# Performance work log

Measured on AMD Instinct MI355X. Metric: run time of the kernel, lower is better.

Reference implementation:

```python
import jax, jax.numpy as jnp
import numpy as np
from jax import lax

IN, H1, H2, OUT = 256, 512, 512, 1
T, B = 2048, 64


def lstm_layer(x, W_ih, W_hh, b_ih, b_hh):
    # x: (T, B, I); W_ih: (4H, I); W_hh: (4H, H); biases: (4H,)
    H = W_hh.shape[1]
    # precompute input contribution for all timesteps (one big GEMM)
    xg = jnp.einsum('tbi,gi->tbg', x, W_ih) + b_ih + b_hh  # (T, B, 4H)

    def step(carry, xg_t):
        h, c = carry
        gates = xg_t + h @ W_hh.T  # (B, 4H), PyTorch gate order i,f,g,o
        i, f, g, o = jnp.split(gates, 4, axis=-1)
        c = jax.nn.sigmoid(f) * c + jax.nn.sigmoid(i) * jnp.tanh(g)
        h = jax.nn.sigmoid(o) * jnp.tanh(c)
        return (h, c), h

    h0 = jnp.zeros((x.shape[1], H), x.dtype)
    _, hs = lax.scan(step, (h0, h0), xg)
    return hs  # (T, B, H)


def setup_inputs() -> dict:
    key = jax.random.key(0)
    ks = jax.random.split(key, 11)
    s1 = 1.0 / np.sqrt(H1)
    s2 = 1.0 / np.sqrt(H2)
    inp = {
        'input': jax.random.normal(ks[0], (T, B, IN), jnp.float32),
        'W_ih1': jax.random.uniform(ks[1], (4 * H1, IN), jnp.float32, -s1, s1),
        'W_hh1': jax.random.uniform(ks[2], (4 * H1, H1), jnp.float32, -s1, s1),
        'b_ih1': jax.random.uniform(ks[3], (4 * H1,), jnp.float32, -s1, s1),
        'b_hh1': jax.random.uniform(ks[4], (4 * H1,), jnp.float32, -s1, s1),
        'W_ih2': jax.random.uniform(ks[5], (4 * H2, H1), jnp.float32, -s2, s2),
        'W_hh2': jax.random.uniform(ks[6], (4 * H2, H2), jnp.float32, -s2, s2),
        'b_ih2': jax.random.uniform(ks[7], (4 * H2,), jnp.float32, -s2, s2),
        'b_hh2': jax.random.uniform(ks[8], (4 * H2,), jnp.float32, -s2, s2),
        'W_out': jax.random.uniform(ks[9], (OUT, H2), jnp.float32, -s2, s2),
        'b_out': jax.random.uniform(ks[10], (OUT,), jnp.float32, -s2, s2),
    }
    return inp


def reference(input, W_ih1, W_hh1, b_ih1, b_hh1, W_ih2, W_hh2, b_ih2, b_hh2, W_out, b_out):
    h1 = lstm_layer(input, W_ih1, W_hh1, b_ih1, b_hh1)   # (T, B, H1)
    h2 = lstm_layer(h1, W_ih2, W_hh2, b_ih2, b_hh2)      # (T, B, H2)
    out = jnp.einsum('tbh,oh->tbo', h2, W_out) + b_out   # (T, B, OUT)
    return jax.nn.sigmoid(out)
```

## Files before the change

kernel.cpp:

```cpp
#include <hip/hip_runtime.h>
#include <math.h>

#define T_STEPS 2048
#define BATCH   64
#define HDIM    512
#define GDIM    2048
#define INDIM   256
#define NBLK_RE 128
#define HB_STEP (HDIM * BATCH)

typedef _Float16 f16x8 __attribute__((ext_vector_type(8)));
typedef _Float16 f16x4 __attribute__((ext_vector_type(4)));
typedef float    f32x4 __attribute__((ext_vector_type(4)));

__device__ __forceinline__ float sigf(float x) { return 1.0f / (1.0f + __expf(-x)); }
__device__ __forceinline__ float tanh_fast(float x) {
    return 1.0f - 2.0f / (__expf(2.0f * x) + 1.0f);
}

__global__ __launch_bounds__(256) void cvt_f16(const float* __restrict__ src,
                                               _Float16* __restrict__ dst, int n4)
{
    int i = blockIdx.x * 256 + threadIdx.x;
    if (i < n4) {
        float4 v = ((const float4*)src)[i];
        f16x4 h;
        h[0] = (_Float16)v.x; h[1] = (_Float16)v.y;
        h[2] = (_Float16)v.z; h[3] = (_Float16)v.w;
        ((f16x4*)dst)[i] = h;
    }
}

__device__ __forceinline__ void wait_flags(const unsigned* __restrict__ flags,
                                           unsigned tgt, int tid)
{
    for (;;) {
        unsigned f = tgt;
        if (tid < NBLK_RE)
            f = __hip_atomic_load(flags + (size_t)tid * 16,
                                  __ATOMIC_RELAXED, __HIP_MEMORY_SCOPE_AGENT);
        if (__syncthreads_and((int)(f >= tgt))) break;
    }
    __atomic_signal_fence(__ATOMIC_ACQUIRE);
}

__global__ __launch_bounds__(256, 1) void lstm_fused(
    const _Float16* __restrict__ xh,
    const _Float16* __restrict__ Wf1h,
    const _Float16* __restrict__ Wf1i,
    const _Float16* __restrict__ Wf2i,
    const _Float16* __restrict__ Wf2h,
    const float* __restrict__ bih1, const float* __restrict__ bhh1,
    const float* __restrict__ bih2, const float* __restrict__ bhh2,
    _Float16* __restrict__ hb1,
    _Float16* __restrict__ hb2,
    float* __restrict__ c1,
    float* __restrict__ c2,
    unsigned* __restrict__ flag1,
    unsigned* __restrict__ flag2,
    int nsteps, unsigned t0a)
{
    __shared__ float    gl[16][68];
    __shared__ _Float16 hsm[64][4];

    const int tid   = threadIdx.x;
    const int layer = blockIdx.x >> 7;
    const int wg    = blockIdx.x & (NBLK_RE - 1);
    const int j0    = wg * 4;
    const int wv    = tid >> 6;
    const int ln    = tid & 63;
    const int l16   = ln & 15;
    const int quad  = ln >> 4;
    const int grow  = (l16 >> 2) * HDIM + j0 + (l16 & 3);
    const int du    = wv;
    const int bu    = tid & 63;
    const int dd    = j0 + du;

    if (layer == 0) {
        f16x8 Bh[16], Bx[8];
#pragma unroll
        for (int j = 0; j < 16; j++) {
            const uint4 u = *(const uint4*)&Wf1h[(size_t)grow * HDIM + j * 32 + quad * 8];
            Bh[j] = __builtin_bit_cast(f16x8, u);
        }
#pragma unroll
        for (int j = 0; j < 8; j++) {
            const uint4 u = *(const uint4*)&Wf1i[(size_t)grow * INDIM + j * 32 + quad * 8];
            Bx[j] = __builtin_bit_cast(f16x8, u);
        }
        float c_reg = c1[(size_t)dd * BATCH + bu];
        const float bi_ = bih1[0 * HDIM + dd] + bhh1[0 * HDIM + dd];
        const float bf_ = bih1[1 * HDIM + dd] + bhh1[1 * HDIM + dd];
        const float bg_ = bih1[2 * HDIM + dd] + bhh1[2 * HDIM + dd];
        const float bo_ = bih1[3 * HDIM + dd] + bhh1[3 * HDIM + dd];

        for (int t = 0; t < nsteps; t++) {
            f32x4 acc0 = {0.f, 0.f, 0.f, 0.f}, acc1 = {0.f, 0.f, 0.f, 0.f};

            {
                const _Float16* xp = xh + ((size_t)t * BATCH + 16 * wv + l16) * INDIM
                                   + quad * 8;
                ulonglong2 ax[8];
#pragma unroll
                for (int j = 0; j < 8; j++)
                    ax[j] = *(const ulonglong2*)(xp + j * 32);
#pragma unroll
                for (int j = 0; j < 8; j += 2) {
                    acc0 = __builtin_amdgcn_mfma_f32_16x16x32_f16(
                        __builtin_bit_cast(f16x8, ax[j]),     Bx[j],     acc0, 0, 0, 0);
                    acc1 = __builtin_amdgcn_mfma_f32_16x16x32_f16(
                        __builtin_bit_cast(f16x8, ax[j + 1]), Bx[j + 1], acc1, 0, 0, 0);
                }
            }

            wait_flags(flag1, t0a + (unsigned)t, tid);
            {
                const _Float16* hp = hb1 + (size_t)t * HB_STEP
                                   + (size_t)(16 * wv + l16) * HDIM + quad * 8;
                ulonglong2 a[16];
#pragma unroll
                for (int j = 0; j < 16; j++)
                    a[j] = *(const ulonglong2*)(hp + j * 32);
#pragma unroll
                for (int j = 0; j < 16; j += 2) {
                    acc0 = __builtin_amdgcn_mfma_f32_16x16x32_f16(
                        __builtin_bit_cast(f16x8, a[j]),     Bh[j],     acc0, 0, 0, 0);
                    acc1 = __builtin_amdgcn_mfma_f32_16x16x32_f16(
                        __builtin_bit_cast(f16x8, a[j + 1]), Bh[j + 1], acc1, 0, 0, 0);
                }
            }
            f32x4 d = acc0 + acc1;
            *(f32x4*)&gl[l16][16 * wv + quad * 4] = d;
            __syncthreads();

            {
                float si = gl[4 * 0 + du][bu] + bi_;
                float sf = gl[4 * 1 + du][bu] + bf_;
                float sg = gl[4 * 2 + du][bu] + bg_;
                float so = gl[4 * 3 + du][bu] + bo_;
                c_reg = sigf(sf) * c_reg + sigf(si) * tanh_fast(sg);
                float h = sigf(so) * tanh_fast(c_reg);
                hsm[bu][du] = (_Float16)h;
            }
            __syncthreads();

            if (tid < 64) {
                unsigned long long pk = *(const unsigned long long*)&hsm[tid][0];
                unsigned long long* dst = (unsigned long long*)
                    (hb1 + (size_t)(t + 1) * HB_STEP + (size_t)tid * HDIM + j0);
                __hip_atomic_store(dst, pk, __ATOMIC_RELAXED, __HIP_MEMORY_SCOPE_AGENT);
                if (t == nsteps - 1) {
                    unsigned long long* dst0 = (unsigned long long*)
                        (hb1 + (size_t)tid * HDIM + j0);
                    __hip_atomic_store(dst0, pk, __ATOMIC_RELAXED, __HIP_MEMORY_SCOPE_AGENT);
                }
                if (tid == 0) {
                    asm volatile("s_waitcnt vmcnt(0)" ::: "memory");
                    __hip_atomic_store(flag1 + (size_t)wg * 16, t0a + (unsigned)t + 1u,
                                       __ATOMIC_RELAXED, __HIP_MEMORY_SCOPE_AGENT);
                }
            }
        }
        c1[(size_t)dd * BATCH + bu] = c_reg;
    } else {
        f16x8 Bh[16], Bi[16];
#pragma unroll
        for (int j = 0; j < 16; j++) {
            const uint4 uh = *(const uint4*)&Wf2h[(size_t)grow * HDIM + j * 32 + quad * 8];
            Bh[j] = __builtin_bit_cast(f16x8, uh);
            const uint4 ui = *(const uint4*)&Wf2i[(size_t)grow * HDIM + j * 32 + quad * 8];
            Bi[j] = __builtin_bit_cast(f16x8, ui);
        }
        float c_reg = c2[(size_t)dd * BATCH + bu];
        const float bi_ = bih2[0 * HDIM + dd] + bhh2[0 * HDIM + dd];
        const float bf_ = bih2[1 * HDIM + dd] + bhh2[1 * HDIM + dd];
        const float bg_ = bih2[2 * HDIM + dd] + bhh2[2 * HDIM + dd];
        const float bo_ = bih2[3 * HDIM + dd] + bhh2[3 * HDIM + dd];

        for (int t = 0; t < nsteps; t++) {
            f32x4 acc0 = {0.f, 0.f, 0.f, 0.f}, acc1 = {0.f, 0.f, 0.f, 0.f};

            wait_flags(flag1, t0a + (unsigned)t + 1u, tid);
            {
                const _Float16* hp = hb1 + (size_t)(t + 1) * HB_STEP
                                   + (size_t)(16 * wv + l16) * HDIM + quad * 8;
                ulonglong2 a[16];
#pragma unroll
                for (int j = 0; j < 16; j++)
                    a[j] = *(const ulonglong2*)(hp + j * 32);
#pragma unroll
                for (int j = 0; j < 16; j += 2) {
                    acc0 = __builtin_amdgcn_mfma_f32_16x16x32_f16(
                        __builtin_bit_cast(f16x8, a[j]),     Bi[j],     acc0, 0, 0, 0);
                    acc1 = __builtin_amdgcn_mfma_f32_16x16x32_f16(
                        __builtin_bit_cast(f16x8, a[j + 1]), Bi[j + 1], acc1, 0, 0, 0);
                }
            }

            wait_flags(flag2, t0a + (unsigned)t, tid);
            {
                const _Float16* hp = hb2 + (size_t)t * HB_STEP
                                   + (size_t)(16 * wv + l16) * HDIM + quad * 8;
                ulonglong2 a[16];
#pragma unroll
                for (int j = 0; j < 16; j++)
                    a[j] = *(const ulonglong2*)(hp + j * 32);
#pragma unroll
                for (int j = 0; j < 16; j += 2) {
                    acc0 = __builtin_amdgcn_mfma_f32_16x16x32_f16(
                        __builtin_bit_cast(f16x8, a[j]),     Bh[j],     acc0, 0, 0, 0);
                    acc1 = __builtin_amdgcn_mfma_f32_16x16x32_f16(
                        __builtin_bit_cast(f16x8, a[j + 1]), Bh[j + 1], acc1, 0, 0, 0);
                }
            }
            f32x4 d = acc0 + acc1;
            *(f32x4*)&gl[l16][16 * wv + quad * 4] = d;
            __syncthreads();

            {
                float si = gl[4 * 0 + du][bu] + bi_;
                float sf = gl[4 * 1 + du][bu] + bf_;
                float sg = gl[4 * 2 + du][bu] + bg_;
                float so = gl[4 * 3 + du][bu] + bo_;
                c_reg = sigf(sf) * c_reg + sigf(si) * tanh_fast(sg);
                float h = sigf(so) * tanh_fast(c_reg);
                hsm[bu][du] = (_Float16)h;
            }
            __syncthreads();

            if (tid < 64) {
                unsigned long long pk = *(const unsigned long long*)&hsm[tid][0];
                unsigned long long* dst = (unsigned long long*)
                    (hb2 + (size_t)(t + 1) * HB_STEP + (size_t)tid * HDIM + j0);
                __hip_atomic_store(dst, pk, __ATOMIC_RELAXED, __HIP_MEMORY_SCOPE_AGENT);
                if (t == nsteps - 1) {
                    unsigned long long* dst0 = (unsigned long long*)
                        (hb2 + (size_t)tid * HDIM + j0);
                    __hip_atomic_store(dst0, pk, __ATOMIC_RELAXED, __HIP_MEMORY_SCOPE_AGENT);
                }
                if (tid == 0) {
                    asm volatile("s_waitcnt vmcnt(0)" ::: "memory");
                    __hip_atomic_store(flag2 + (size_t)wg * 16, t0a + (unsigned)t + 1u,
                                       __ATOMIC_RELAXED, __HIP_MEMORY_SCOPE_AGENT);
                }
            }
        }
        c2[(size_t)dd * BATCH + bu] = c_reg;
    }
}

__global__ __launch_bounds__(256) void out_kernel(
    const _Float16* __restrict__ h2, const float* __restrict__ Wout,
    const float* __restrict__ bout, float* __restrict__ out)
{
    const int t = blockIdx.x;
    const int q = threadIdx.x >> 6, b = threadIdx.x & 63;
    const _Float16* base = &h2[(size_t)t * HB_STEP + (size_t)b * HDIM];
    float s = 0.0f;
#pragma unroll 8
    for (int k = q * 128; k < q * 128 + 128; k += 4) {
        const uint2 u = *(const uint2*)&base[k];
        f16x4 h = __builtin_bit_cast(f16x4, u);
        s += Wout[k] * (float)h[0] + Wout[k + 1] * (float)h[1]
           + Wout[k + 2] * (float)h[2] + Wout[k + 3] * (float)h[3];
    }
    __shared__ float red[4][64];
    red[q][b] = s;
    __syncthreads();
    if (q == 0) {
        float v = red[0][b] + red[1][b] + red[2][b] + red[3][b] + bout[0];
        out[t * BATCH + b] = sigf(v);
    }
}

static size_t req_bytes(int C) {
    return 65536
         + 2ull * HDIM * BATCH * 4
         + 3ull * GDIM * HDIM * 2
         + (size_t)GDIM * INDIM * 2
         + (size_t)T_STEPS * BATCH * INDIM * 2
         + 2ull * (size_t)(C + 1) * BATCH * HDIM * 2;
}

extern "C" void kernel_launch(void* const* d_in, const int* in_sizes, int n_in,
                              void* d_out, int out_size, void* d_ws, size_t ws_size,
                              hipStream_t stream)
{
    const float* x    = (const float*)d_in[0];
    const float* Wih1 = (const float*)d_in[1];
    const float* Whh1 = (const float*)d_in[2];
    const float* bih1 = (const float*)d_in[3];
    const float* bhh1 = (const float*)d_in[4];
    const float* Wih2 = (const float*)d_in[5];
    const float* Whh2 = (const float*)d_in[6];
    const float* bih2 = (const float*)d_in[7];
    const float* bhh2 = (const float*)d_in[8];
    const float* Wout = (const float*)d_in[9];
    const float* bout = (const float*)d_in[10];
    float* out = (float*)d_out;

    int C = 8;
    const int cands[] = {2048, 1024, 512, 256, 128, 64, 32, 16, 8};
    for (int i = 0; i < 9; i++)
        if (req_bytes(cands[i]) <= ws_size) { C = cands[i]; break; }

    char* p = (char*)d_ws;
    unsigned*  flag1 = (unsigned*)p;                p += 32768;
    unsigned*  flag2 = (unsigned*)p;                p += 32768;
    float*     c1    = (float*)p;                   p += (size_t)HDIM * BATCH * 4;
    float*     c2    = (float*)p;                   p += (size_t)HDIM * BATCH * 4;
    _Float16*  Wf1h  = (_Float16*)p;                p += (size_t)GDIM * HDIM * 2;
    _Float16*  Wf1i  = (_Float16*)p;                p += (size_t)GDIM * INDIM * 2;
    _Float16*  Wf2i  = (_Float16*)p;                p += (size_t)GDIM * HDIM * 2;
    _Float16*  Wf2h  = (_Float16*)p;                p += (size_t)GDIM * HDIM * 2;
    _Float16*  xh    = (_Float16*)p;                p += (size_t)T_STEPS * BATCH * INDIM * 2;
    _Float16*  hb1   = (_Float16*)p;                p += (size_t)(C + 1) * BATCH * HDIM * 2;
    _Float16*  hb2   = (_Float16*)p;

    hipMemsetAsync(flag1, 0, 65536 + 2ull * HDIM * BATCH * 4, stream);
    hipMemsetAsync(hb1, 0, (size_t)BATCH * HDIM * 2, stream);
    hipMemsetAsync(hb2, 0, (size_t)BATCH * HDIM * 2, stream);

    cvt_f16<<<dim3(GDIM * HDIM / 4 / 256), dim3(256), 0, stream>>>(Whh1, Wf1h, GDIM * HDIM / 4);
    cvt_f16<<<dim3(GDIM * INDIM / 4 / 256), dim3(256), 0, stream>>>(Wih1, Wf1i, GDIM * INDIM / 4);
    cvt_f16<<<dim3(GDIM * HDIM / 4 / 256), dim3(256), 0, stream>>>(Wih2, Wf2i, GDIM * HDIM / 4);
    cvt_f16<<<dim3(GDIM * HDIM / 4 / 256), dim3(256), 0, stream>>>(Whh2, Wf2h, GDIM * HDIM / 4);
    cvt_f16<<<dim3(T_STEPS * BATCH * INDIM / 4 / 256), dim3(256), 0, stream>>>(
        x, xh, T_STEPS * BATCH * INDIM / 4);

    const _Float16* h2r = hb2 + (size_t)HB_STEP;

    for (int t0 = 0; t0 < T_STEPS; t0 += C) {
        const _Float16* xc = xh + (size_t)t0 * BATCH * INDIM;
        unsigned t0a = (unsigned)t0;
        void* args[] = {(void*)&xc, (void*)&Wf1h, (void*)&Wf1i, (void*)&Wf2i,
                        (void*)&Wf2h, (void*)&bih1, (void*)&bhh1, (void*)&bih2,
                        (void*)&bhh2, (void*)&hb1, (void*)&hb2, (void*)&c1,
                        (void*)&c2, (void*)&flag1, (void*)&flag2, (void*)&C,
                        (void*)&t0a};
        hipLaunchCooperativeKernel((void*)lstm_fused, dim3(2 * NBLK_RE), dim3(256),
                                   args, 0, stream);

        out_kernel<<<dim3(C), dim3(256), 0, stream>>>(h2r, Wout, bout,
                                                      out + (size_t)t0 * BATCH);
    }

    (void)in_sizes; (void)n_in; (void)out_size;
}
```

Before: 13.22 ms.

## Precompute layer-1 input gates per chunk and switch to single atomic counter barriers

Moves the layer-1 input projection (x·W_ih + biases) out of the recurrent loop into a separate MFMA GEMM kernel that writes fp16 gate preactivations per chunk. The recurrent kernel then only does the h·W_hh product for layer 1, reading the precomputed gates. The per-block flag array polled by 128 threads is replaced by one shared atomic counter per layer per chunk, incremented with fetch_add and spun on by every thread. This shortens the serial critical path per step, but it adds an extra kernel launch per chunk, rounds the input gates to fp16, and concentrates contention on a single atomic address.

```diff
diff --git a/kernel.cpp b/kernel.cpp
--- a/kernel.cpp
+++ b/kernel.cpp
@@ -31,34 +31,69 @@
     }
 }
 
-__device__ __forceinline__ void wait_flags(const unsigned* __restrict__ flags,
-                                           unsigned tgt, int tid)
-{
-    for (;;) {
-        unsigned f = tgt;
-        if (tid < NBLK_RE)
-            f = __hip_atomic_load(flags + (size_t)tid * 16,
-                                  __ATOMIC_RELAXED, __HIP_MEMORY_SCOPE_AGENT);
-        if (__syncthreads_and((int)(f >= tgt))) break;
-    }
-    __atomic_signal_fence(__ATOMIC_ACQUIRE);
+__global__ __launch_bounds__(256) void gemm_xg_mfma(
+    const _Float16* __restrict__ xh,
+    const _Float16* __restrict__ Wfi,
+    const float* __restrict__ b1, const float* __restrict__ b2,
+    _Float16* __restrict__ xg, int nsteps)
+{
+    const int wg   = blockIdx.x;
+    const int j0   = wg * 4;
+    const int tid  = threadIdx.x;
+    const int wv   = tid >> 6;
+    const int ln   = tid & 63;
+    const int l16  = ln & 15;
+    const int quad = ln >> 4;
+    const int grow = (l16 >> 2) * HDIM + j0 + (l16 & 3);
+
+    f16x8 Bx[8];
+#pragma unroll
+    for (int j = 0; j < 8; j++) {
+        const uint4 u = *(const uint4*)&Wfi[(size_t)grow * INDIM + j * 32 + quad * 8];
+        Bx[j] = __builtin_bit_cast(f16x8, u);
+    }
+    const float bias = b1[grow] + b2[grow];
+
+    const int ts = nsteps >> 3;
+    const int t0 = blockIdx.y * ts;
+    for (int t = t0; t < t0 + ts; t++) {
+        const _Float16* xp = xh + ((size_t)t * BATCH + 16 * wv + l16) * INDIM
+                           + quad * 8;
+        ulonglong2 a[8];
+#pragma unroll
+        for (int j = 0; j < 8; j++)
+            a[j] = *(const ulonglong2*)(xp + j * 32);
+        f32x4 acc0 = {0.f, 0.f, 0.f, 0.f}, acc1 = {0.f, 0.f, 0.f, 0.f};
+#pragma unroll
+        for (int j = 0; j < 8; j += 2) {
+            acc0 = __builtin_amdgcn_mfma_f32_16x16x32_f16(
+                __builtin_bit_cast(f16x8, a[j]),     Bx[j],     acc0, 0, 0, 0);
+            acc1 = __builtin_amdgcn_mfma_f32_16x16x32_f16(
+                __builtin_bit_cast(f16x8, a[j + 1]), Bx[j + 1], acc1, 0, 0, 0);
+        }
+        f32x4 d = acc0 + acc1;
+        f16x4 o;
+#pragma unroll
+        for (int r = 0; r < 4; r++) o[r] = (_Float16)(d[r] + bias);
+        *(uint2*)&xg[((size_t)t * GDIM + grow) * BATCH + 16 * wv + quad * 4]
+            = __builtin_bit_cast(uint2, o);
+    }
 }
 
 __global__ __launch_bounds__(256, 1) void lstm_fused(
-    const _Float16* __restrict__ xh,
-    const _Float16* __restrict__ Wf1h,
-    const _Float16* __restrict__ Wf1i,
+    const _Float16* __restrict__ xg,
+    const _Float16* __restrict__ Wf1,
     const _Float16* __restrict__ Wf2i,
     const _Float16* __restrict__ Wf2h,
-    const float* __restrict__ bih1, const float* __restrict__ bhh1,
-    const float* __restrict__ bih2, const float* __restrict__ bhh2,
+    const float* __restrict__ bih2,
+    const float* __restrict__ bhh2,
     _Float16* __restrict__ hb1,
     _Float16* __restrict__ hb2,
     float* __restrict__ c1,
     float* __restrict__ c2,
-    unsigned* __restrict__ flag1,
-    unsigned* __restrict__ flag2,
-    int nsteps, unsigned t0a)
+    unsigned* __restrict__ ctr1,
+    unsigned* __restrict__ ctr2,
+    int nsteps)
 {
     __shared__ float    gl[16][68];
     __shared__ _Float16 hsm[64][4];
@@ -74,70 +109,57 @@
     const int grow  = (l16 >> 2) * HDIM + j0 + (l16 & 3);
     const int du    = wv;
     const int bu    = tid & 63;
-    const int dd    = j0 + du;
 
     if (layer == 0) {
-        f16x8 Bh[16], Bx[8];
+        f16x8 Bf[16];
 #pragma unroll
         for (int j = 0; j < 16; j++) {
-            const uint4 u = *(const uint4*)&Wf1h[(size_t)grow * HDIM + j * 32 + quad * 8];
-            Bh[j] = __builtin_bit_cast(f16x8, u);
-        }
-#pragma unroll
-        for (int j = 0; j < 8; j++) {
-            const uint4 u = *(const uint4*)&Wf1i[(size_t)grow * INDIM + j * 32 + quad * 8];
-            Bx[j] = __builtin_bit_cast(f16x8, u);
-        }
-        float c_reg = c1[(size_t)dd * BATCH + bu];
-        const float bi_ = bih1[0 * HDIM + dd] + bhh1[0 * HDIM + dd];
-        const float bf_ = bih1[1 * HDIM + dd] + bhh1[1 * HDIM + dd];
-        const float bg_ = bih1[2 * HDIM + dd] + bhh1[2 * HDIM + dd];
-        const float bo_ = bih1[3 * HDIM + dd] + bhh1[3 * HDIM + dd];
+            const uint4 u = *(const uint4*)&Wf1[(size_t)grow * HDIM + j * 32 + quad * 8];
+            Bf[j] = __builtin_bit_cast(f16x8, u);
+        }
+        float c_reg = c1[(size_t)(j0 + du) * BATCH + bu];
+
+        const size_t xo0 = (size_t)(0 * HDIM + j0 + du) * BATCH + bu;
+        const size_t xo1 = (size_t)(1 * HDIM + j0 + du) * BATCH + bu;
+        const size_t xo2 = (size_t)(2 * HDIM + j0 + du) * BATCH + bu;
+        const size_t xo3 = (size_t)(3 * HDIM + j0 + du) * BATCH + bu;
 
         for (int t = 0; t < nsteps; t++) {
+            const _Float16* xgt = xg + (size_t)t * GDIM * BATCH;
+            float x0 = (float)xgt[xo0], x1 = (float)xgt[xo1];
+            float x2 = (float)xgt[xo2], x3 = (float)xgt[xo3];
+
+            if (t > 0) {
+                const unsigned tgt = (unsigned)(NBLK_RE * t);
+                while (__hip_atomic_load(ctr1, __ATOMIC_RELAXED,
+                                         __HIP_MEMORY_SCOPE_AGENT) < tgt) {}
+                __atomic_signal_fence(__ATOMIC_ACQUIRE);
+            }
+
+            const _Float16* hp = hb1 + (size_t)t * HB_STEP
+                               + (size_t)(16 * wv + l16) * HDIM + quad * 8;
+            ulonglong2 a[16];
+#pragma unroll
+            for (int j = 0; j < 16; j++)
+                a[j] = *(const ulonglong2*)(hp + j * 32);
+
             f32x4 acc0 = {0.f, 0.f, 0.f, 0.f}, acc1 = {0.f, 0.f, 0.f, 0.f};
-
-            {
-                const _Float16* xp = xh + ((size_t)t * BATCH + 16 * wv + l16) * INDIM
-                                   + quad * 8;
-                ulonglong2 ax[8];
-#pragma unroll
-                for (int j = 0; j < 8; j++)
-                    ax[j] = *(const ulonglong2*)(xp + j * 32);
-#pragma unroll
-                for (int j = 0; j < 8; j += 2) {
-                    acc0 = __builtin_amdgcn_mfma_f32_16x16x32_f16(
-                        __builtin_bit_cast(f16x8, ax[j]),     Bx[j],     acc0, 0, 0, 0);
-                    acc1 = __builtin_amdgcn_mfma_f32_16x16x32_f16(
-                        __builtin_bit_cast(f16x8, ax[j + 1]), Bx[j + 1], acc1, 0, 0, 0);
-                }
-            }
-
-            wait_flags(flag1, t0a + (unsigned)t, tid);
-            {
-                const _Float16* hp = hb1 + (size_t)t * HB_STEP
-                                   + (size_t)(16 * wv + l16) * HDIM + quad * 8;
-                ulonglong2 a[16];
-#pragma unroll
-                for (int j = 0; j < 16; j++)
-                    a[j] = *(const ulonglong2*)(hp + j * 32);
-#pragma unroll
-                for (int j = 0; j < 16; j += 2) {
-                    acc0 = __builtin_amdgcn_mfma_f32_16x16x32_f16(
-                        __builtin_bit_cast(f16x8, a[j]),     Bh[j],     acc0, 0, 0, 0);
-                    acc1 = __builtin_amdgcn_mfma_f32_16x16x32_f16(
-                        __builtin_bit_cast(f16x8, a[j + 1]), Bh[j + 1], acc1, 0, 0, 0);
-                }
+#pragma unroll
+            for (int j = 0; j < 16; j += 2) {
+                acc0 = __builtin_amdgcn_mfma_f32_16x16x32_f16(
+                    __builtin_bit_cast(f16x8, a[j]),     Bf[j],     acc0, 0, 0, 0);
+                acc1 = __builtin_amdgcn_mfma_f32_16x16x32_f16(
+                    __builtin_bit_cast(f16x8, a[j + 1]), Bf[j + 1], acc1, 0, 0, 0);
             }
             f32x4 d = acc0 + acc1;
             *(f32x4*)&gl[l16][16 * wv + quad * 4] = d;
             __syncthreads();
 
             {
-                float si = gl[4 * 0 + du][bu] + bi_;
-                float sf = gl[4 * 1 + du][bu] + bf_;
-                float sg = gl[4 * 2 + du][bu] + bg_;
-                float so = gl[4 * 3 + du][bu] + bo_;
+                float si = gl[4 * 0 + du][bu] + x0;
+                float sf = gl[4 * 1 + du][bu] + x1;
+                float sg = gl[4 * 2 + du][bu] + x2;
+                float so = gl[4 * 3 + du][bu] + x3;
                 c_reg = sigf(sf) * c_reg + sigf(si) * tanh_fast(sg);
                 float h = sigf(so) * tanh_fast(c_reg);
                 hsm[bu][du] = (_Float16)h;
@@ -156,12 +178,12 @@
                 }
                 if (tid == 0) {
                     asm volatile("s_waitcnt vmcnt(0)" ::: "memory");
-                    __hip_atomic_store(flag1 + (size_t)wg * 16, t0a + (unsigned)t + 1u,
-                                       __ATOMIC_RELAXED, __HIP_MEMORY_SCOPE_AGENT);
-                }
-            }
-        }
-        c1[(size_t)dd * BATCH + bu] = c_reg;
+                    __hip_atomic_fetch_add(ctr1, 1u, __ATOMIC_RELAXED,
+                                           __HIP_MEMORY_SCOPE_AGENT);
+                }
+            }
+        }
+        c1[(size_t)(j0 + du) * BATCH + bu] = c_reg;
     } else {
         f16x8 Bh[16], Bi[16];
 #pragma unroll
@@ -171,7 +193,8 @@
             const uint4 ui = *(const uint4*)&Wf2i[(size_t)grow * HDIM + j * 32 + quad * 8];
             Bi[j] = __builtin_bit_cast(f16x8, ui);
         }
-        float c_reg = c2[(size_t)dd * BATCH + bu];
+        float c_reg = c2[(size_t)(j0 + du) * BATCH + bu];
+        const int dd = j0 + du;
         const float bi_ = bih2[0 * HDIM + dd] + bhh2[0 * HDIM + dd];
         const float bf_ = bih2[1 * HDIM + dd] + bhh2[1 * HDIM + dd];
         const float bg_ = bih2[2 * HDIM + dd] + bhh2[2 * HDIM + dd];
@@ -180,7 +203,12 @@
         for (int t = 0; t < nsteps; t++) {
             f32x4 acc0 = {0.f, 0.f, 0.f, 0.f}, acc1 = {0.f, 0.f, 0.f, 0.f};
 
-            wait_flags(flag1, t0a + (unsigned)t + 1u, tid);
+            {
+                const unsigned tgt = (unsigned)(NBLK_RE * (t + 1));
+                while (__hip_atomic_load(ctr1, __ATOMIC_RELAXED,
+                                         __HIP_MEMORY_SCOPE_AGENT) < tgt) {}
+                __atomic_signal_fence(__ATOMIC_ACQUIRE);
+            }
             {
                 const _Float16* hp = hb1 + (size_t)(t + 1) * HB_STEP
                                    + (size_t)(16 * wv + l16) * HDIM + quad * 8;
@@ -197,7 +225,12 @@
                 }
             }
 
-            wait_flags(flag2, t0a + (unsigned)t, tid);
+            if (t > 0) {
+                const unsigned tgt = (unsigned)(NBLK_RE * t);
+                while (__hip_atomic_load(ctr2, __ATOMIC_RELAXED,
+                                         __HIP_MEMORY_SCOPE_AGENT) < tgt) {}
+                __atomic_signal_fence(__ATOMIC_ACQUIRE);
+            }
             {
                 const _Float16* hp = hb2 + (size_t)t * HB_STEP
                                    + (size_t)(16 * wv + l16) * HDIM + quad * 8;
@@ -240,12 +273,12 @@
                 }
                 if (tid == 0) {
                     asm volatile("s_waitcnt vmcnt(0)" ::: "memory");
-                    __hip_atomic_store(flag2 + (size_t)wg * 16, t0a + (unsigned)t + 1u,
-                                       __ATOMIC_RELAXED, __HIP_MEMORY_SCOPE_AGENT);
-                }
-            }
-        }
-        c2[(size_t)dd * BATCH + bu] = c_reg;
+                    __hip_atomic_fetch_add(ctr2, 1u, __ATOMIC_RELAXED,
+                                           __HIP_MEMORY_SCOPE_AGENT);
+                }
+            }
+        }
+        c2[(size_t)(j0 + du) * BATCH + bu] = c_reg;
     }
 }
 
@@ -274,12 +307,13 @@
 }
 
 static size_t req_bytes(int C) {
-    return 65536
+    return 4096
          + 2ull * HDIM * BATCH * 4
          + 3ull * GDIM * HDIM * 2
          + (size_t)GDIM * INDIM * 2
          + (size_t)T_STEPS * BATCH * INDIM * 2
-         + 2ull * (size_t)(C + 1) * BATCH * HDIM * 2;
+         + 2ull * (size_t)(C + 1) * BATCH * HDIM * 2
+         + (size_t)C * GDIM * BATCH * 2;
 }
 
 extern "C" void kernel_launch(void* const* d_in, const int* in_sizes, int n_in,
@@ -299,14 +333,13 @@
     const float* bout = (const float*)d_in[10];
     float* out = (float*)d_out;
 
-    int C = 8;
-    const int cands[] = {2048, 1024, 512, 256, 128, 64, 32, 16, 8};
-    for (int i = 0; i < 9; i++)
+    int C = 256;
+    const int cands[] = {2048, 1024, 512, 256};
+    for (int i = 0; i < 4; i++)
         if (req_bytes(cands[i]) <= ws_size) { C = cands[i]; break; }
 
     char* p = (char*)d_ws;
-    unsigned*  flag1 = (unsigned*)p;                p += 32768;
-    unsigned*  flag2 = (unsigned*)p;                p += 32768;
+    unsigned*  ctr   = (unsigned*)p;                p += 4096;
     float*     c1    = (float*)p;                   p += (size_t)HDIM * BATCH * 4;
     float*     c2    = (float*)p;                   p += (size_t)HDIM * BATCH * 4;
     _Float16*  Wf1h  = (_Float16*)p;                p += (size_t)GDIM * HDIM * 2;
@@ -315,9 +348,10 @@
     _Float16*  Wf2h  = (_Float16*)p;                p += (size_t)GDIM * HDIM * 2;
     _Float16*  xh    = (_Float16*)p;                p += (size_t)T_STEPS * BATCH * INDIM * 2;
     _Float16*  hb1   = (_Float16*)p;                p += (size_t)(C + 1) * BATCH * HDIM * 2;
-    _Float16*  hb2   = (_Float16*)p;
-
-    hipMemsetAsync(flag1, 0, 65536 + 2ull * HDIM * BATCH * 4, stream);
+    _Float16*  hb2   = (_Float16*)p;                p += (size_t)(C + 1) * BATCH * HDIM * 2;
+    _Float16*  xg    = (_Float16*)p;
+
+    hipMemsetAsync(ctr, 0, 4096 + 2ull * HDIM * BATCH * 4, stream);
     hipMemsetAsync(hb1, 0, (size_t)BATCH * HDIM * 2, stream);
     hipMemsetAsync(hb2, 0, (size_t)BATCH * HDIM * 2, stream);
 
@@ -329,15 +363,18 @@
         x, xh, T_STEPS * BATCH * INDIM / 4);
 
     const _Float16* h2r = hb2 + (size_t)HB_STEP;
-
-    for (int t0 = 0; t0 < T_STEPS; t0 += C) {
+    int cidx = 0;
+
+    for (int t0 = 0; t0 < T_STEPS; t0 += C, cidx++) {
         const _Float16* xc = xh + (size_t)t0 * BATCH * INDIM;
-        unsigned t0a = (unsigned)t0;
-        void* args[] = {(void*)&xc, (void*)&Wf1h, (void*)&Wf1i, (void*)&Wf2i,
-                        (void*)&Wf2h, (void*)&bih1, (void*)&bhh1, (void*)&bih2,
-                        (void*)&bhh2, (void*)&hb1, (void*)&hb2, (void*)&c1,
-                        (void*)&c2, (void*)&flag1, (void*)&flag2, (void*)&C,
-                        (void*)&t0a};
+        gemm_xg_mfma<<<dim3(NBLK_RE, 8), dim3(256), 0, stream>>>(
+            xc, Wf1i, bih1, bhh1, xg, C);
+
+        unsigned* c1p = ctr + (size_t)cidx * 64;
+        unsigned* c2p = c1p + 32;
+        void* args[] = {(void*)&xg, (void*)&Wf1h, (void*)&Wf2i, (void*)&Wf2h,
+                        (void*)&bih2, (void*)&bhh2, (void*)&hb1, (void*)&hb2,
+                        (void*)&c1, (void*)&c2, (void*)&c1p, (void*)&c2p, (void*)&C};
         hipLaunchCooperativeKernel((void*)lstm_fused, dim3(2 * NBLK_RE), dim3(256),
                                    args, 0, stream);
 
```

Result: slower. 18.21 ms (+37.8%).
